# Kernel tuning notes

Measured on AMD Instinct MI355X. Metric: run time of the kernel, lower is better.

Reference implementation:

```python
import jax, jax.numpy as jnp
import numpy as np

SHAPE = (32, 512, 512)  # (D, H, W) dense voxel grid
N_ACTIVE = 150000


def setup_inputs() -> dict:
    key = jax.random.key(0)
    k_f, k_w1, k_w2 = jax.random.split(key, 3)
    D, H, W = SHAPE
    # unique active voxel coordinates (collision-free dense-grid hash)
    rng = np.random.default_rng(0)
    lin = rng.permutation(D * H * W)[:N_ACTIVE]
    z = lin // (H * W)
    y = (lin // W) % H
    x = lin % W
    coors = np.stack([np.zeros(N_ACTIVE, np.int32), z.astype(np.int32),
                      y.astype(np.int32), x.astype(np.int32)], axis=1)
    features = jax.random.normal(k_f, (N_ACTIVE, 3), dtype=jnp.float32)
    # per-offset GEMM weights: [K^3, Cin, Cout]
    w1 = jax.random.normal(k_w1, (27, 3, 128), dtype=jnp.float32) * 0.2
    w2 = jax.random.normal(k_w2, (27, 128, 128), dtype=jnp.float32) * 0.05
    return {"features": features, "coors": jnp.asarray(coors), "w1": w1,
            "w2": w2, "batch_size": 1}


def _build_grid(coors):
    D, H, W = SHAPE
    n = coors.shape[0]
    grid = jnp.full((D, H, W), -1, dtype=jnp.int32)
    return grid.at[coors[:, 1], coors[:, 2], coors[:, 3]].set(
        jnp.arange(n, dtype=jnp.int32))


def _subm_conv3d(feat, coors, grid, w):
    """Submanifold 3x3x3 conv: gather active neighbors per offset, GEMM, accumulate.
    feat: [N, Cin]; w: [27, Cin, Cout]; output defined only on active sites -> [N, Cout]."""
    D, H, W = SHAPE
    n = feat.shape[0]
    out = jnp.zeros((n, w.shape[-1]), dtype=feat.dtype)
    k = 0
    for dz in (-1, 0, 1):
        for dy in (-1, 0, 1):
            for dx in (-1, 0, 1):
                nz = coors[:, 1] + dz
                ny = coors[:, 2] + dy
                nx = coors[:, 3] + dx
                inb = ((nz >= 0) & (nz < D) & (ny >= 0) & (ny < H)
                       & (nx >= 0) & (nx < W))
                nidx = grid[jnp.clip(nz, 0, D - 1), jnp.clip(ny, 0, H - 1),
                            jnp.clip(nx, 0, W - 1)]
                valid = inb & (nidx >= 0)
                g = jnp.where(valid[:, None],
                              feat[jnp.clip(nidx, 0, n - 1)], 0.0)  # [N, Cin]
                out = out + g @ w[k]
                k += 1
    return out


def reference(features, coors, w1, w2, batch_size):
    # SparseConvTensor: features [N,3], coors [N,4] (batch,z,y,x), batch_size=1
    grid = _build_grid(coors)
    h = _subm_conv3d(features, coors, grid, w1)   # SubMConv3d(3, 128, 3)
    out = _subm_conv3d(h, coors, grid, w2)        # SubMConv3d(128, 128, 3), shared indice_key
    return out
```

## Files before the change

### kernel.cpp

```cpp
#include <hip/hip_runtime.h>
#include <stdint.h>

#define GD 32
#define GH 512
#define GW 512
#define GDHW (GD * GH * GW)
#define KOFF 27
#define CAP 4096
#define CNTS 32
#define NW2 (KOFF * 128 * 128)

typedef __attribute__((ext_vector_type(8))) short short8;
typedef __attribute__((ext_vector_type(4))) float f32x4;

__device__ __forceinline__ unsigned short f32_to_bf16(float x) {
    unsigned int u = __float_as_uint(x);
    unsigned int r = (u + 0x7FFFu + ((u >> 16) & 1u)) >> 16;
    return (unsigned short)r;
}

__global__ __launch_bounds__(256) void setup_kernel(
    const int* __restrict__ coors, int* __restrict__ grid,
    unsigned int* __restrict__ bitgrid,
    const float* __restrict__ w2, unsigned short* __restrict__ w2t,
    int n, int nbsc) {
    const int bid = blockIdx.x, t = threadIdx.x;
    if (bid < nbsc) {
        int i = bid * 256 + t;
        if (i < n) {
            int z = coors[i * 4 + 1];
            int y = coors[i * 4 + 2];
            int x = coors[i * 4 + 3];
            int cell = (z * GH + y) * GW + x;
            grid[cell] = i;
            atomicOr(&bitgrid[cell >> 5], 1u << (cell & 31));
        }
    } else {
        int g = (bid - nbsc) * 256 + t;
        if (g < NW2) {
            int k = g >> 14;
            int c = (g >> 7) & 127;
            int q = g & 127;
            w2t[g] = f32_to_bf16(w2[(k * 128 + q) * 128 + c]);
        }
    }
}

__global__ __launch_bounds__(256) void nbr1_kernel(
    const int* __restrict__ coors, const int* __restrict__ grid,
    const unsigned int* __restrict__ bitgrid,
    int* __restrict__ vcnt, int* __restrict__ nbrc,
    unsigned long long* __restrict__ wmask, int* __restrict__ bcnt,
    int n, int nb) {
    __shared__ int wcnt[4][26];

    const int bid = blockIdx.x;
    const int i = bid * 256 + threadIdx.x;
    const int t = threadIdx.x, wave = t >> 6, lane = t & 63;
    const bool live = (i < n);

    int z = 0, y = 0, x = 0;
    if (live) {
        z = coors[i * 4 + 1];
        y = coors[i * 4 + 2];
        x = coors[i * 4 + 3];
    }

    int j[27];
#pragma unroll
    for (int k = 0; k < 27; ++k) {
        if (k == 13) { j[k] = live ? i : -1; continue; }
        int dz = k / 9 - 1, dy = (k / 3) % 3 - 1, dx = k % 3 - 1;
        int nz = z + dz, ny = y + dy, nx = x + dx;
        int cz = min(max(nz, 0), GD - 1);
        int cy = min(max(ny, 0), GH - 1);
        int cx = min(max(nx, 0), GW - 1);
        int cell = (cz * GH + cy) * GW + cx;
        bool ok = live && nz >= 0 && nz < GD && ny >= 0 && ny < GH &&
                  nx >= 0 && nx < GW;
        unsigned int word = bitgrid[cell >> 5];
        bool occ = ok && ((word >> (cell & 31)) & 1u);
        j[k] = occ ? grid[cell] : -1;
    }

    if (live) {
        int c = 0;
#pragma unroll
        for (int k = 0; k < 27; ++k) {
            if (k == 13) continue;
            if (j[k] >= 0) { nbrc[i * 27 + c] = (k << 20) | j[k]; ++c; }
        }
        vcnt[i] = c;
    }

#pragma unroll
    for (int kk = 0; kk < 26; ++kk) {
        const int k = kk + (kk >= 13);
        unsigned long long m = __ballot(live && (j[k] >= 0));
        if (lane == 0) {
            wmask[((size_t)bid * 4 + wave) * 26 + kk] = m;
            wcnt[wave][kk] = __popcll(m);
        }
    }
    __syncthreads();
    if (t < 26)
        bcnt[t * nb + bid] = wcnt[0][t] + wcnt[1][t] + wcnt[2][t] + wcnt[3][t];
}

__global__ __launch_bounds__(256) void scan_kernel(
    const int* __restrict__ bcnt, int* __restrict__ bbase,
    int* __restrict__ cnts, int nb) {
    const int k = blockIdx.x;
    const int t = threadIdx.x;
    __shared__ int s[256];
    int run = 0;
    for (int base = 0; base < nb; base += 256) {
        int idx = base + t;
        int v = (idx < nb) ? bcnt[k * nb + idx] : 0;
        s[t] = v;
        __syncthreads();
        for (int off = 1; off < 256; off <<= 1) {
            int u = (t >= off) ? s[t - off] : 0;
            __syncthreads();
            s[t] += u;
            __syncthreads();
        }
        int incl = s[t];
        int total = s[255];
        if (idx < nb) bbase[k * nb + idx] = run + incl - v;
        run += total;
        __syncthreads();
    }
    if (t == 0) cnts[k * CNTS] = run;
}

__global__ __launch_bounds__(256) void nbr2_kernel(
    const int* __restrict__ vcnt, const int* __restrict__ nbrc,
    const unsigned long long* __restrict__ wmask,
    const int* __restrict__ bbase,
    int* __restrict__ pairs, int* __restrict__ npos, int n, int nb) {
    __shared__ unsigned long long lmsk[4][26];
    __shared__ int woff[4][26];
    __shared__ int bb[26];

    const int bid = blockIdx.x;
    const int t = threadIdx.x, wave = t >> 6, lane = t & 63;
    if (t < 26) {
        unsigned long long m0 = wmask[((size_t)bid * 4 + 0) * 26 + t];
        unsigned long long m1 = wmask[((size_t)bid * 4 + 1) * 26 + t];
        unsigned long long m2 = wmask[((size_t)bid * 4 + 2) * 26 + t];
        unsigned long long m3 = wmask[((size_t)bid * 4 + 3) * 26 + t];
        lmsk[0][t] = m0; lmsk[1][t] = m1; lmsk[2][t] = m2; lmsk[3][t] = m3;
        int p0 = __popcll(m0), p1 = __popcll(m1), p2 = __popcll(m2);
        woff[0][t] = 0; woff[1][t] = p0; woff[2][t] = p0 + p1;
        woff[3][t] = p0 + p1 + p2;
        bb[t] = bbase[t * nb + bid];
    }
    __syncthreads();

    const int i = bid * 256 + t;
    if (i >= n) return;
    const unsigned long long lmask = (1ull << lane) - 1;
    const int cnt = vcnt[i];
    for (int s = 0; s < cnt; ++s) {
        int e = nbrc[i * 27 + s];
        int k = e >> 20, j = e & 0xFFFFF;
        int kk = k - (k > 13);
        int pos = bb[kk] + woff[wave][kk] + __popcll(lmsk[wave][kk] & lmask);
        if (pos < CAP) {
            pairs[kk * CAP + pos] = j;
            npos[i * 27 + s] = kk * CAP + pos;
        } else {
            npos[i * 27 + s] = -1;
        }
    }
}

__global__ __launch_bounds__(256) void conv1_kernel(
    const float* __restrict__ feat, const float* __restrict__ w1,
    const int* __restrict__ vcnt, const int* __restrict__ nbrc,
    unsigned short* __restrict__ hout, int n) {
    const int wave = threadIdx.x >> 6, lane = threadIdx.x & 63;
    const int i = blockIdx.x * 4 + wave;
    if (i >= n) return;
    const int c2 = lane * 2;

    const int cnt = vcnt[i];
    float f0 = feat[i * 3 + 0];
    float f1 = feat[i * 3 + 1];
    float f2 = feat[i * 3 + 2];

    const float* wc = w1 + 13 * 384 + c2;
    float2 w0 = *(const float2*)(wc);
    float2 wv1 = *(const float2*)(wc + 128);
    float2 w2_ = *(const float2*)(wc + 256);
    float a0 = f0 * w0.x + f1 * wv1.x + f2 * w2_.x;
    float a1 = f0 * w0.y + f1 * wv1.y + f2 * w2_.y;

    for (int s = 0; s < cnt; ++s) {
        int e = nbrc[i * 27 + s];
        int k = e >> 20, jj = e & 0xFFFFF;
        float g0 = feat[jj * 3 + 0];
        float g1 = feat[jj * 3 + 1];
        float g2 = feat[jj * 3 + 2];
        const float* wk = w1 + k * 384 + c2;
        float2 u0 = *(const float2*)(wk);
        float2 u1 = *(const float2*)(wk + 128);
        float2 u2 = *(const float2*)(wk + 256);
        a0 += g0 * u0.x + g1 * u1.x + g2 * u2.x;
        a1 += g0 * u0.y + g1 * u1.y + g2 * u2.y;
    }

    unsigned int packed = (unsigned int)f32_to_bf16(a0) |
                          ((unsigned int)f32_to_bf16(a1) << 16);
    *(unsigned int*)(hout + (size_t)i * 128 + c2) = packed;
}

__global__ __launch_bounds__(256, 2) void conv2a_kernel(
    const unsigned short* __restrict__ h,
    const unsigned short* __restrict__ w2t,
    float* __restrict__ out, int n) {
    const int t = threadIdx.x;
    const int wave = t >> 6, lane = t & 63;
    const int lane16 = lane & 15, quad = lane >> 4;
    const int wm = wave >> 1, wn = wave & 1;
    const int row0 = blockIdx.x * 128;

    short8 a[4][4];
#pragma unroll
    for (int ms = 0; ms < 4; ++ms) {
        int r = row0 + wm * 64 + ms * 16 + lane16;
        r = min(r, n - 1);
        const unsigned short* hp = h + (size_t)r * 128 + quad * 8;
#pragma unroll
        for (int ks = 0; ks < 4; ++ks)
            a[ms][ks] = *(const short8*)(hp + ks * 32);
    }

    short8 b[4][4];
    const unsigned short* wbase = w2t + 13 * 16384 + quad * 8;
#pragma unroll
    for (int ns = 0; ns < 4; ++ns) {
        int c = wn * 64 + ns * 16 + lane16;
        const unsigned short* wp = wbase + c * 128;
#pragma unroll
        for (int ks = 0; ks < 4; ++ks)
            b[ns][ks] = *(const short8*)(wp + ks * 32);
    }

    f32x4 acc[4][4];
#pragma unroll
    for (int p = 0; p < 4; ++p)
#pragma unroll
        for (int q = 0; q < 4; ++q) acc[p][q] = (f32x4){0.f, 0.f, 0.f, 0.f};

#pragma unroll
    for (int ks = 0; ks < 4; ++ks)
#pragma unroll
        for (int ns = 0; ns < 4; ++ns)
#pragma unroll
            for (int ms = 0; ms < 4; ++ms)
                acc[ms][ns] = __builtin_amdgcn_mfma_f32_16x16x32_bf16(
                    a[ms][ks], b[ns][ks], acc[ms][ns], 0, 0, 0);

#pragma unroll
    for (int ms = 0; ms < 4; ++ms) {
#pragma unroll
        for (int r = 0; r < 4; ++r) {
            int i = row0 + wm * 64 + ms * 16 + quad * 4 + r;
            if (i < n) {
#pragma unroll
                for (int ns = 0; ns < 4; ++ns) {
                    int col = wn * 64 + ns * 16 + lane16;
                    out[(size_t)i * 128 + col] = acc[ms][ns][r];
                }
            }
        }
    }
}

__global__ __launch_bounds__(256, 2) void conv2b_kernel(
    const unsigned short* __restrict__ h,
    const unsigned short* __restrict__ w2t,
    const int* __restrict__ pairs, const int* __restrict__ cnts,
    unsigned short* __restrict__ corr) {
    const int kb = blockIdx.x >> 5;
    const int tile = blockIdx.x & 31;
    const int cnt = min(cnts[kb * CNTS], CAP);
    const int base = tile * 128;
    if (base >= cnt) return;
    const int m = min(128, cnt - base);
    const int k = kb + (kb >= 13);
    const int* pk = pairs + kb * CAP + base;

    const int t = threadIdx.x;
    const int wave = t >> 6, lane = t & 63;
    const int lane16 = lane & 15, quad = lane >> 4;
    const int wm = wave >> 1, wn = wave & 1;

    short8 a[4][4];
#pragma unroll
    for (int ms = 0; ms < 4; ++ms) {
        int r = wm * 64 + ms * 16 + lane16;
        bool v = (r < m);
        int j = v ? pk[r] : 0;
        const unsigned short* hp = h + (size_t)j * 128 + quad * 8;
#pragma unroll
        for (int ks = 0; ks < 4; ++ks)
            a[ms][ks] = v ? *(const short8*)(hp + ks * 32)
                          : (short8){0, 0, 0, 0, 0, 0, 0, 0};
    }

    short8 b[4][4];
    const unsigned short* wbase = w2t + (size_t)k * 16384 + quad * 8;
#pragma unroll
    for (int ns = 0; ns < 4; ++ns) {
        int c = wn * 64 + ns * 16 + lane16;
        const unsigned short* wp = wbase + c * 128;
#pragma unroll
        for (int ks = 0; ks < 4; ++ks)
            b[ns][ks] = *(const short8*)(wp + ks * 32);
    }

    f32x4 acc[4][4];
#pragma unroll
    for (int p = 0; p < 4; ++p)
#pragma unroll
        for (int q = 0; q < 4; ++q) acc[p][q] = (f32x4){0.f, 0.f, 0.f, 0.f};

#pragma unroll
    for (int ks = 0; ks < 4; ++ks)
#pragma unroll
        for (int ns = 0; ns < 4; ++ns)
#pragma unroll
            for (int ms = 0; ms < 4; ++ms)
                acc[ms][ns] = __builtin_amdgcn_mfma_f32_16x16x32_bf16(
                    a[ms][ks], b[ns][ks], acc[ms][ns], 0, 0, 0);

#pragma unroll
    for (int ms = 0; ms < 4; ++ms) {
#pragma unroll
        for (int r = 0; r < 4; ++r) {
            int row = wm * 64 + ms * 16 + quad * 4 + r;
            if (row < m) {
                unsigned short* cr =
                    corr + (size_t)(kb * CAP + base + row) * 128;
#pragma unroll
                for (int ns = 0; ns < 4; ++ns) {
                    int col = wn * 64 + ns * 16 + lane16;
                    cr[col] = f32_to_bf16(acc[ms][ns][r]);
                }
            }
        }
    }
}

__global__ __launch_bounds__(256) void fixup_kernel(
    const unsigned short* __restrict__ corr, const int* __restrict__ vcnt,
    const int* __restrict__ npos, float* __restrict__ out, int n) {
    const int i = blockIdx.x * 4 + (threadIdx.x >> 6);
    const int lane = threadIdx.x & 63;
    if (i >= n) return;
    const int cnt = vcnt[i];
    if (cnt == 0) return;
    const int* np = npos + i * 27;

    float a0 = 0.f, a1 = 0.f;
    for (int s = 0; s < cnt; ++s) {
        int p = np[s];
        if (p >= 0) {
            unsigned int u =
                *(const unsigned int*)(corr + (size_t)p * 128 + lane * 2);
            a0 += __uint_as_float(u << 16);
            a1 += __uint_as_float(u & 0xFFFF0000u);
        }
    }
    float2* op = (float2*)(out + (size_t)i * 128) + lane;
    float2 cur = *op;
    cur.x += a0;
    cur.y += a1;
    *op = cur;
}

extern "C" void kernel_launch(void* const* d_in, const int* in_sizes, int n_in,
                              void* d_out, int out_size, void* d_ws,
                              size_t ws_size, hipStream_t stream) {
    const float* feat = (const float*)d_in[0];
    const int* coors = (const int*)d_in[1];
    const float* w1 = (const float*)d_in[2];
    const float* w2 = (const float*)d_in[3];
    float* out = (float*)d_out;

    const int n = in_sizes[0] / 3;
    const int nb = (n + 255) / 256;

    uint8_t* ws = (uint8_t*)d_ws;
    size_t off = 0;
    int* grid = (int*)(ws + off); off += (size_t)GDHW * 4;
    unsigned int* bitgrid = (unsigned int*)(ws + off);
    off += (size_t)(GDHW / 8);
    int* vcnt = (int*)(ws + off); off += (size_t)n * 4;
    int* nbrc = (int*)(ws + off); off += (size_t)n * 27 * 4;
    int* npos = (int*)(ws + off); off += (size_t)n * 27 * 4;
    off = (off + 255) & ~(size_t)255;
    unsigned long long* wmask = (unsigned long long*)(ws + off);
    off += (size_t)nb * 4 * 26 * 8;
    int* bcnt = (int*)(ws + off); off += (size_t)26 * nb * 4;
    int* bbase = (int*)(ws + off); off += (size_t)26 * nb * 4;
    off = (off + 255) & ~(size_t)255;
    unsigned short* hbuf = (unsigned short*)(ws + off);
    off += (size_t)n * 128 * 2;
    off = (off + 255) & ~(size_t)255;
    unsigned short* w2t = (unsigned short*)(ws + off);
    off += (size_t)KOFF * 128 * 128 * 2;
    off = (off + 255) & ~(size_t)255;
    int* pairs = (int*)(ws + off);
    off += (size_t)26 * CAP * 4;
    off = (off + 255) & ~(size_t)255;
    int* cnts = (int*)(ws + off); off += 26 * CNTS * 4;
    off = (off + 255) & ~(size_t)255;
    unsigned short* corr = (unsigned short*)(ws + off);
    off += (size_t)26 * CAP * 128 * 2;

    hipMemsetAsync(bitgrid, 0x00, (size_t)(GDHW / 8), stream);

    const int nbw2 = (NW2 + 255) / 256;
    setup_kernel<<<nb + nbw2, 256, 0, stream>>>(coors, grid, bitgrid, w2, w2t,
                                                n, nb);
    nbr1_kernel<<<nb, 256, 0, stream>>>(coors, grid, bitgrid, vcnt, nbrc,
                                        wmask, bcnt, n, nb);
    scan_kernel<<<26, 256, 0, stream>>>(bcnt, bbase, cnts, nb);
    nbr2_kernel<<<nb, 256, 0, stream>>>(vcnt, nbrc, wmask, bbase, pairs, npos,
                                        n, nb);
    conv1_kernel<<<(n + 3) / 4, 256, 0, stream>>>(feat, w1, vcnt, nbrc, hbuf, n);
    conv2b_kernel<<<26 * 32, 256, 0, stream>>>(hbuf, w2t, pairs, cnts, corr);
    conv2a_kernel<<<(n + 127) / 128, 256, 0, stream>>>(hbuf, w2t, out, n);
    fixup_kernel<<<(n + 3) / 4, 256, 0, stream>>>(corr, vcnt, npos, out, n);
}
```

Measured before the change: 246.5 us.

## Merge scan with conv1 and conv2a with conv2b; share bitgrid words per row

Neighbor lookup now loads two bitgrid words per (dz,dy) row instead of one per offset, and reads grid only for occupied cells. It builds a compact per-voxel occupancy mask for the ballots instead of keeping the 27-entry index array. The scan kernel and conv1 are merged into one launch via block-index dispatch, as are the pair-list GEMM (conv2b) and the center-offset GEMM (conv2a). This removes two launches and lets independent work overlap, at the cost of more complex kernels whose register use is set by the larger branch.

```diff
diff --git a/kernel.cpp b/kernel.cpp
--- a/kernel.cpp
+++ b/kernel.cpp
@@ -66,37 +66,48 @@
         x = coors[i * 4 + 3];
     }
 
-    int j[27];
-#pragma unroll
-    for (int k = 0; k < 27; ++k) {
-        if (k == 13) { j[k] = live ? i : -1; continue; }
-        int dz = k / 9 - 1, dy = (k / 3) % 3 - 1, dx = k % 3 - 1;
-        int nz = z + dz, ny = y + dy, nx = x + dx;
+    int c0r[9];
+    bool rowok[9];
+    unsigned int wlo[9], whi[9];
+#pragma unroll
+    for (int r = 0; r < 9; ++r) {
+        int dz = r / 3 - 1, dy = r % 3 - 1;
+        int nz = z + dz, ny = y + dy;
         int cz = min(max(nz, 0), GD - 1);
         int cy = min(max(ny, 0), GH - 1);
-        int cx = min(max(nx, 0), GW - 1);
-        int cell = (cz * GH + cy) * GW + cx;
-        bool ok = live && nz >= 0 && nz < GD && ny >= 0 && ny < GH &&
-                  nx >= 0 && nx < GW;
-        unsigned int word = bitgrid[cell >> 5];
-        bool occ = ok && ((word >> (cell & 31)) & 1u);
-        j[k] = occ ? grid[cell] : -1;
-    }
-
-    if (live) {
-        int c = 0;
-#pragma unroll
-        for (int k = 0; k < 27; ++k) {
-            if (k == 13) continue;
-            if (j[k] >= 0) { nbrc[i * 27 + c] = (k << 20) | j[k]; ++c; }
-        }
-        vcnt[i] = c;
-    }
+        int c0 = (cz * GH + cy) * GW + x;
+        c0r[r] = c0;
+        rowok[r] = live && nz >= 0 && nz < GD && ny >= 0 && ny < GH;
+        wlo[r] = bitgrid[(c0 - 1) >> 5];
+        whi[r] = bitgrid[(c0 + 1) >> 5];
+    }
+
+    unsigned int mask26 = 0;
+    int c = 0;
+#pragma unroll
+    for (int k = 0; k < 27; ++k) {
+        if (k == 13) continue;
+        int r = k / 3, dx = k % 3 - 1;
+        int nx = x + dx;
+        int cell = c0r[r] + dx;
+        bool ok = rowok[r] && nx >= 0 && nx < GW;
+        unsigned int w;
+        if (dx < 0) w = wlo[r];
+        else if (dx > 0) w = whi[r];
+        else w = ((cell & 31) == 0) ? whi[r] : wlo[r];
+        bool occ = ok && ((w >> (cell & 31)) & 1u);
+        if (occ) {
+            int jj = grid[cell];
+            nbrc[i * 27 + c] = (k << 20) | jj;
+            ++c;
+            mask26 |= 1u << (k - (k > 13));
+        }
+    }
+    if (live) vcnt[i] = c;
 
 #pragma unroll
     for (int kk = 0; kk < 26; ++kk) {
-        const int k = kk + (kk >= 13);
-        unsigned long long m = __ballot(live && (j[k] >= 0));
+        unsigned long long m = __ballot((mask26 >> kk) & 1u);
         if (lane == 0) {
             wmask[((size_t)bid * 4 + wave) * 26 + kk] = m;
             wcnt[wave][kk] = __popcll(m);
@@ -107,31 +118,71 @@
         bcnt[t * nb + bid] = wcnt[0][t] + wcnt[1][t] + wcnt[2][t] + wcnt[3][t];
 }
 
-__global__ __launch_bounds__(256) void scan_kernel(
+__global__ __launch_bounds__(256) void scan_conv1_kernel(
     const int* __restrict__ bcnt, int* __restrict__ bbase,
-    int* __restrict__ cnts, int nb) {
-    const int k = blockIdx.x;
+    int* __restrict__ cnts, int nb,
+    const float* __restrict__ feat, const float* __restrict__ w1,
+    const int* __restrict__ vcnt, const int* __restrict__ nbrc,
+    unsigned short* __restrict__ hout, int n) {
     const int t = threadIdx.x;
-    __shared__ int s[256];
-    int run = 0;
-    for (int base = 0; base < nb; base += 256) {
-        int idx = base + t;
-        int v = (idx < nb) ? bcnt[k * nb + idx] : 0;
-        s[t] = v;
-        __syncthreads();
-        for (int off = 1; off < 256; off <<= 1) {
-            int u = (t >= off) ? s[t - off] : 0;
+    if (blockIdx.x < 26) {
+        const int k = blockIdx.x;
+        __shared__ int s[256];
+        int run = 0;
+        for (int base = 0; base < nb; base += 256) {
+            int idx = base + t;
+            int v = (idx < nb) ? bcnt[k * nb + idx] : 0;
+            s[t] = v;
             __syncthreads();
-            s[t] += u;
+            for (int off = 1; off < 256; off <<= 1) {
+                int u = (t >= off) ? s[t - off] : 0;
+                __syncthreads();
+                s[t] += u;
+                __syncthreads();
+            }
+            int incl = s[t];
+            int total = s[255];
+            if (idx < nb) bbase[k * nb + idx] = run + incl - v;
+            run += total;
             __syncthreads();
         }
-        int incl = s[t];
-        int total = s[255];
-        if (idx < nb) bbase[k * nb + idx] = run + incl - v;
-        run += total;
-        __syncthreads();
-    }
-    if (t == 0) cnts[k * CNTS] = run;
+        if (t == 0) cnts[k * CNTS] = run;
+        return;
+    }
+    const int wave = t >> 6, lane = t & 63;
+    const int i = (blockIdx.x - 26) * 4 + wave;
+    if (i >= n) return;
+    const int c2 = lane * 2;
+
+    const int cnt = vcnt[i];
+    float f0 = feat[i * 3 + 0];
+    float f1 = feat[i * 3 + 1];
+    float f2 = feat[i * 3 + 2];
+
+    const float* wc = w1 + 13 * 384 + c2;
+    float2 w0 = *(const float2*)(wc);
+    float2 wv1 = *(const float2*)(wc + 128);
+    float2 w2_ = *(const float2*)(wc + 256);
+    float a0 = f0 * w0.x + f1 * wv1.x + f2 * w2_.x;
+    float a1 = f0 * w0.y + f1 * wv1.y + f2 * w2_.y;
+
+    for (int s = 0; s < cnt; ++s) {
+        int e = nbrc[i * 27 + s];
+        int k = e >> 20, jj = e & 0xFFFFF;
+        float g0 = feat[jj * 3 + 0];
+        float g1 = feat[jj * 3 + 1];
+        float g2 = feat[jj * 3 + 2];
+        const float* wk = w1 + k * 384 + c2;
+        float2 u0 = *(const float2*)(wk);
+        float2 u1 = *(const float2*)(wk + 128);
+        float2 u2 = *(const float2*)(wk + 256);
+        a0 += g0 * u0.x + g1 * u1.x + g2 * u2.x;
+        a1 += g0 * u0.y + g1 * u1.y + g2 * u2.y;
+    }
+
+    unsigned int packed = (unsigned int)f32_to_bf16(a0) |
+                          ((unsigned int)f32_to_bf16(a1) << 16);
+    *(unsigned int*)(hout + (size_t)i * 128 + c2) = packed;
 }
 
 __global__ __launch_bounds__(256) void nbr2_kernel(
@@ -176,55 +227,86 @@
     }
 }
 
-__global__ __launch_bounds__(256) void conv1_kernel(
-    const float* __restrict__ feat, const float* __restrict__ w1,
-    const int* __restrict__ vcnt, const int* __restrict__ nbrc,
-    unsigned short* __restrict__ hout, int n) {
-    const int wave = threadIdx.x >> 6, lane = threadIdx.x & 63;
-    const int i = blockIdx.x * 4 + wave;
-    if (i >= n) return;
-    const int c2 = lane * 2;
-
-    const int cnt = vcnt[i];
-    float f0 = feat[i * 3 + 0];
-    float f1 = feat[i * 3 + 1];
-    float f2 = feat[i * 3 + 2];
-
-    const float* wc = w1 + 13 * 384 + c2;
-    float2 w0 = *(const float2*)(wc);
-    float2 wv1 = *(const float2*)(wc + 128);
-    float2 w2_ = *(const float2*)(wc + 256);
-    float a0 = f0 * w0.x + f1 * wv1.x + f2 * w2_.x;
-    float a1 = f0 * w0.y + f1 * wv1.y + f2 * w2_.y;
-
-    for (int s = 0; s < cnt; ++s) {
-        int e = nbrc[i * 27 + s];
-        int k = e >> 20, jj = e & 0xFFFFF;
-        float g0 = feat[jj * 3 + 0];
-        float g1 = feat[jj * 3 + 1];
-        float g2 = feat[jj * 3 + 2];
-        const float* wk = w1 + k * 384 + c2;
-        float2 u0 = *(const float2*)(wk);
-        float2 u1 = *(const float2*)(wk + 128);
-        float2 u2 = *(const float2*)(wk + 256);
-        a0 += g0 * u0.x + g1 * u1.x + g2 * u2.x;
-        a1 += g0 * u0.y + g1 * u1.y + g2 * u2.y;
-    }
-
-    unsigned int packed = (unsigned int)f32_to_bf16(a0) |
-                          ((unsigned int)f32_to_bf16(a1) << 16);
-    *(unsigned int*)(hout + (size_t)i * 128 + c2) = packed;
-}
-
-__global__ __launch_bounds__(256, 2) void conv2a_kernel(
+__global__ __launch_bounds__(256, 2) void conv2ab_kernel(
     const unsigned short* __restrict__ h,
     const unsigned short* __restrict__ w2t,
+    const int* __restrict__ pairs, const int* __restrict__ cnts,
+    unsigned short* __restrict__ corr,
     float* __restrict__ out, int n) {
     const int t = threadIdx.x;
     const int wave = t >> 6, lane = t & 63;
     const int lane16 = lane & 15, quad = lane >> 4;
     const int wm = wave >> 1, wn = wave & 1;
-    const int row0 = blockIdx.x * 128;
+
+    if (blockIdx.x < 26 * 32) {
+        const int kb = blockIdx.x >> 5;
+        const int tile = blockIdx.x & 31;
+        const int cnt = min(cnts[kb * CNTS], CAP);
+        const int base = tile * 128;
+        if (base >= cnt) return;
+        const int m = min(128, cnt - base);
+        const int k = kb + (kb >= 13);
+        const int* pk = pairs + kb * CAP + base;
+
+        short8 a[4][4];
+#pragma unroll
+        for (int ms = 0; ms < 4; ++ms) {
+            int r = wm * 64 + ms * 16 + lane16;
+            bool v = (r < m);
+            int j = v ? pk[r] : 0;
+            const unsigned short* hp = h + (size_t)j * 128 + quad * 8;
+#pragma unroll
+            for (int ks = 0; ks < 4; ++ks)
+                a[ms][ks] = v ? *(const short8*)(hp + ks * 32)
+                              : (short8){0, 0, 0, 0, 0, 0, 0, 0};
+        }
+
+        short8 b[4][4];
+        const unsigned short* wbase = w2t + (size_t)k * 16384 + quad * 8;
+#pragma unroll
+        for (int ns = 0; ns < 4; ++ns) {
+            int c = wn * 64 + ns * 16 + lane16;
+            const unsigned short* wp = wbase + c * 128;
+#pragma unroll
+            for (int ks = 0; ks < 4; ++ks)
+                b[ns][ks] = *(const short8*)(wp + ks * 32);
+        }
+
+        f32x4 acc[4][4];
+#pragma unroll
+        for (int p = 0; p < 4; ++p)
+#pragma unroll
+            for (int q = 0; q < 4; ++q) acc[p][q] = (f32x4){0.f, 0.f, 0.f, 0.f};
+
+#pragma unroll
+        for (int ks = 0; ks < 4; ++ks)
+#pragma unroll
+            for (int ns = 0; ns < 4; ++ns)
+#pragma unroll
+                for (int ms = 0; ms < 4; ++ms)
+                    acc[ms][ns] = __builtin_amdgcn_mfma_f32_16x16x32_bf16(
+                        a[ms][ks], b[ns][ks], acc[ms][ns], 0, 0, 0);
+
+#pragma unroll
+        for (int ms = 0; ms < 4; ++ms) {
+#pragma unroll
+            for (int r = 0; r < 4; ++r) {
+                int row = wm * 64 + ms * 16 + quad * 4 + r;
+                if (row < m) {
+                    unsigned short* cr =
+                        corr + (size_t)(kb * CAP + base + row) * 128;
+#pragma unroll
+                    for (int ns = 0; ns < 4; ++ns) {
+                        int col = wn * 64 + ns * 16 + lane16;
+                        cr[col] = f32_to_bf16(acc[ms][ns][r]);
+                    }
+                }
+            }
+        }
+        return;
+    }
+
+    const int row0 = (blockIdx.x - 26 * 32) * 128;
 
     short8 a[4][4];
 #pragma unroll
@@ -273,82 +355,6 @@
                 for (int ns = 0; ns < 4; ++ns) {
                     int col = wn * 64 + ns * 16 + lane16;
                     out[(size_t)i * 128 + col] = acc[ms][ns][r];
-                }
-            }
-        }
-    }
-}
-
-__global__ __launch_bounds__(256, 2) void conv2b_kernel(
-    const unsigned short* __restrict__ h,
-    const unsigned short* __restrict__ w2t,
-    const int* __restrict__ pairs, const int* __restrict__ cnts,
-    unsigned short* __restrict__ corr) {
-    const int kb = blockIdx.x >> 5;
-    const int tile = blockIdx.x & 31;
-    const int cnt = min(cnts[kb * CNTS], CAP);
-    const int base = tile * 128;
-    if (base >= cnt) return;
-    const int m = min(128, cnt - base);
-    const int k = kb + (kb >= 13);
-    const int* pk = pairs + kb * CAP + base;
-
-    const int t = threadIdx.x;
-    const int wave = t >> 6, lane = t & 63;
-    const int lane16 = lane & 15, quad = lane >> 4;
-    const int wm = wave >> 1, wn = wave & 1;
-
-    short8 a[4][4];
-#pragma unroll
-    for (int ms = 0; ms < 4; ++ms) {
-        int r = wm * 64 + ms * 16 + lane16;
-        bool v = (r < m);
-        int j = v ? pk[r] : 0;
-        const unsigned short* hp = h + (size_t)j * 128 + quad * 8;
-#pragma unroll
-        for (int ks = 0; ks < 4; ++ks)
-            a[ms][ks] = v ? *(const short8*)(hp + ks * 32)
-                          : (short8){0, 0, 0, 0, 0, 0, 0, 0};
-    }
-
-    short8 b[4][4];
-    const unsigned short* wbase = w2t + (size_t)k * 16384 + quad * 8;
-#pragma unroll
-    for (int ns = 0; ns < 4; ++ns) {
-        int c = wn * 64 + ns * 16 + lane16;
-        const unsigned short* wp = wbase + c * 128;
-#pragma unroll
-        for (int ks = 0; ks < 4; ++ks)
-            b[ns][ks] = *(const short8*)(wp + ks * 32);
-    }
-
-    f32x4 acc[4][4];
-#pragma unroll
-    for (int p = 0; p < 4; ++p)
-#pragma unroll
-        for (int q = 0; q < 4; ++q) acc[p][q] = (f32x4){0.f, 0.f, 0.f, 0.f};
-
-#pragma unroll
-    for (int ks = 0; ks < 4; ++ks)
-#pragma unroll
-        for (int ns = 0; ns < 4; ++ns)
-#pragma unroll
-            for (int ms = 0; ms < 4; ++ms)
-                acc[ms][ns] = __builtin_amdgcn_mfma_f32_16x16x32_bf16(
-                    a[ms][ks], b[ns][ks], acc[ms][ns], 0, 0, 0);
-
-#pragma unroll
-    for (int ms = 0; ms < 4; ++ms) {
-#pragma unroll
-        for (int r = 0; r < 4; ++r) {
-            int row = wm * 64 + ms * 16 + quad * 4 + r;
-            if (row < m) {
-                unsigned short* cr =
-                    corr + (size_t)(kb * CAP + base + row) * 128;
-#pragma unroll
-                for (int ns = 0; ns < 4; ++ns) {
-                    int col = wn * 64 + ns * 16 + lane16;
-                    cr[col] = f32_to_bf16(acc[ms][ns][r]);
                 }
             }
         }
@@ -429,11 +435,11 @@
                                                 n, nb);
     nbr1_kernel<<<nb, 256, 0, stream>>>(coors, grid, bitgrid, vcnt, nbrc,
                                         wmask, bcnt, n, nb);
-    scan_kernel<<<26, 256, 0, stream>>>(bcnt, bbase, cnts, nb);
+    scan_conv1_kernel<<<26 + (n + 3) / 4, 256, 0, stream>>>(
+        bcnt, bbase, cnts, nb, feat, w1, vcnt, nbrc, hbuf, n);
     nbr2_kernel<<<nb, 256, 0, stream>>>(vcnt, nbrc, wmask, bbase, pairs, npos,
                                         n, nb);
-    conv1_kernel<<<(n + 3) / 4, 256, 0, stream>>>(feat, w1, vcnt, nbrc, hbuf, n);
-    conv2b_kernel<<<26 * 32, 256, 0, stream>>>(hbuf, w2t, pairs, cnts, corr);
-    conv2a_kernel<<<(n + 127) / 128, 256, 0, stream>>>(hbuf, w2t, out, n);
+    conv2ab_kernel<<<26 * 32 + (n + 127) / 128, 256, 0, stream>>>(
+        hbuf, w2t, pairs, cnts, corr, out, n);
     fixup_kernel<<<(n + 3) / 4, 256, 0, stream>>>(corr, vcnt, npos, out, n);
 }
```

Result: faster. 228.2 us (-7.4%).
